# Optimization experiments

Measured on AMD Instinct MI355X. Metric: run time of the kernel, lower is better.

## Reference

```python
import jax, jax.numpy as jnp
import numpy as np

E, H, L = 1280, 20, 8192
D = E // H


def setup_inputs() -> dict:
    key = jax.random.key(0)
    ks = jax.random.split(key, 12)
    inp = {
        "hidden_states": jax.random.normal(ks[0], (1, 1, E), jnp.float32),
        "position_ids": jax.random.randint(ks[1], (1,), 0, L, jnp.int64),
        "k_cache": jax.random.normal(ks[2], (1, H, L, D), jnp.float32),
        "v_cache": jax.random.normal(ks[3], (1, H, L, D), jnp.float32),
        "Wq": jax.random.normal(ks[4], (E, E), jnp.float32) * 0.02,
        "bq": jax.random.normal(ks[5], (E,), jnp.float32) * 0.02,
        "Wk": jax.random.normal(ks[6], (E, E), jnp.float32) * 0.02,
        "Wv": jax.random.normal(ks[7], (E, E), jnp.float32) * 0.02,
        "bv": jax.random.normal(ks[8], (E,), jnp.float32) * 0.02,
        "Wo": jax.random.normal(ks[9], (E, E), jnp.float32) * 0.02,
        "bo": jax.random.normal(ks[10], (E,), jnp.float32) * 0.02,
    }
    return inp


def reference(hidden_states, position_ids, k_cache, v_cache, Wq, bq, Wk, Wv, bv, Wo, bo):
    # hidden_states: [1,1,E]; k_cache/v_cache: [1,H,L,D]; position_ids: [1] int
    h = k_cache.shape[1]
    d = k_cache.shape[3]
    l = k_cache.shape[2]
    e = h * d
    scale = jnp.asarray(d, hidden_states.dtype) ** -0.5

    def split_heads(x):  # [1,1,E] -> [1,H,1,D]
        return x.reshape(1, 1, h, d).transpose(0, 2, 1, 3)

    q = split_heads((hidden_states @ Wq.T + bq) * scale)
    k_new = split_heads(hidden_states @ Wk.T)          # k_proj has no bias
    v_new = split_heads(hidden_states @ Wv.T + bv)

    pos = position_ids.reshape(())
    positions = jnp.arange(l)
    write_mask = (positions == pos)[None, None, :, None]   # [1,1,L,1]
    # masked broadcast-update of the KV cache (same math as cache*(1-m)+new*m)
    new_k_cache = jnp.where(write_mask, k_new, k_cache)    # [1,H,L,D]
    new_v_cache = jnp.where(write_mask, v_new, v_cache)

    scores = jnp.einsum('bhqd,bhkd->bhqk', q, new_k_cache)  # [1,H,1,L]
    causal = jnp.where(positions[None, None, None, :] <= pos,
                       jnp.asarray(0.0, scores.dtype),
                       jnp.asarray(-1e9, scores.dtype))
    attn = jax.nn.softmax(scores + causal, axis=-1)
    out = jnp.einsum('bhqk,bhkd->bhqd', attn, new_v_cache)  # [1,H,1,D]
    out = out.transpose(0, 2, 1, 3).reshape(1, 1, e)
    out = out @ Wo.T + bo
    return out, new_k_cache, new_v_cache
```

## Files before the change

### kernel.cpp

```cpp
#include <hip/hip_runtime.h>

#define E 1280
#define H 20
#define L 8192
#define D 64
#define CHUNK 128
#define NCHUNK (L / CHUNK)

typedef float f4 __attribute__((ext_vector_type(4)));

__global__ void qkv_kernel(const float* __restrict__ hs,
                           const float* __restrict__ Wq, const float* __restrict__ bq,
                           const float* __restrict__ Wk,
                           const float* __restrict__ Wv, const float* __restrict__ bv,
                           float* __restrict__ qkv) {
    int row_global = blockIdx.x * 4 + (threadIdx.x >> 6);
    int lane = threadIdx.x & 63;
    int mat = row_global / E;
    int row = row_global - mat * E;
    const float* W = (mat == 0) ? Wq : (mat == 1) ? Wk : Wv;
    const float4* Wrow = (const float4*)(W + (size_t)row * E);
    const float4* h4 = (const float4*)hs;
    float sum = 0.f;
#pragma unroll
    for (int i = 0; i < 5; ++i) {
        int idx = lane + 64 * i;
        float4 w4 = Wrow[idx];
        float4 x4 = h4[idx];
        sum += w4.x * x4.x + w4.y * x4.y + w4.z * x4.z + w4.w * x4.w;
    }
#pragma unroll
    for (int off = 32; off > 0; off >>= 1) sum += __shfl_down(sum, off, 64);
    if (lane == 0) {
        float val;
        if (mat == 0)      val = (sum + bq[row]) * 0.125f;
        else if (mat == 1) val = sum;
        else               val = sum + bv[row];
        qkv[mat * E + row] = val;
    }
}

__global__ void kv_kernel(const float* __restrict__ kc, const float* __restrict__ vc,
                          const float* __restrict__ qkv, const int* __restrict__ pos_p,
                          float* __restrict__ out_k, float* __restrict__ out_v,
                          float* __restrict__ cmax, float* __restrict__ csum,
                          float* __restrict__ o_part) {
    int h = blockIdx.x / NCHUNK;
    int c = blockIdx.x - h * NCHUNK;
    int pos = pos_p[0];
    int tid = threadIdx.x;
    int wave = tid >> 6;
    int lane = tid & 63;
    int cc = tid & 15;
    int rg = tid >> 4;

    __shared__ float s_part[CHUNK][17];
    __shared__ float s_w[CHUNK];
    __shared__ float smax4[4];
    __shared__ float spsum[4];
    __shared__ float sacc[4][D];

    float4 q4  = ((const float4*)qkv)[h * 16 + cc];
    float4 kn4 = ((const float4*)(qkv + E))[h * 16 + cc];
    float4 vn4 = ((const float4*)(qkv + 2 * E))[h * 16 + cc];

    size_t base = ((size_t)h * L + (size_t)c * CHUNK) * D;
    const float* kbase = kc + base;
    const float* vbase = vc + base;
    float* okbase = out_k + base;
    float* ovbase = out_v + base;
    int l0 = c * CHUNK;

#pragma unroll
    for (int it = 0; it < CHUNK / 16; ++it) {
        int r = it * 16 + rg;
        int l = l0 + r;
        float4 k4 = ((const float4*)(kbase + r * D))[cc];
        if (l == pos) k4 = kn4;
        f4 kv = {k4.x, k4.y, k4.z, k4.w};
        __builtin_nontemporal_store(kv, (f4*)(okbase + r * D) + cc);
        s_part[r][cc] = k4.x * q4.x + k4.y * q4.y + k4.z * q4.z + k4.w * q4.w;
    }

    float4 vreg[CHUNK / 16];
#pragma unroll
    for (int it = 0; it < CHUNK / 16; ++it) {
        int r = it * 16 + rg;
        int l = l0 + r;
        float4 v4 = ((const float4*)(vbase + r * D))[cc];
        if (l == pos) v4 = vn4;
        f4 vv = {v4.x, v4.y, v4.z, v4.w};
        __builtin_nontemporal_store(vv, (f4*)(ovbase + r * D) + cc);
        vreg[it] = v4;
    }
    __syncthreads();

    float s = -INFINITY;
    if (tid < CHUNK) {
        float sum = 0.f;
#pragma unroll
        for (int i = 0; i < 16; ++i) sum += s_part[tid][i];
        s = (l0 + tid <= pos) ? sum : -INFINITY;
    }
    float lm = s;
#pragma unroll
    for (int off = 32; off > 0; off >>= 1)
        lm = fmaxf(lm, __shfl_xor(lm, off, 64));
    if (lane == 0) smax4[wave] = lm;
    __syncthreads();
    float m = fmaxf(fmaxf(smax4[0], smax4[1]), fmaxf(smax4[2], smax4[3]));

    float p = 0.f;
    if (tid < CHUNK) {
        p = (s > -1e30f) ? __expf(s - m) : 0.f;
        s_w[tid] = p;
    }
    float ps = p;
#pragma unroll
    for (int off = 32; off > 0; off >>= 1) ps += __shfl_xor(ps, off, 64);
    if (lane == 0) spsum[wave] = ps;
    __syncthreads();

    float4 acc = {0.f, 0.f, 0.f, 0.f};
#pragma unroll
    for (int it = 0; it < CHUNK / 16; ++it) {
        int r = it * 16 + rg;
        float w = s_w[r];
        acc.x += w * vreg[it].x; acc.y += w * vreg[it].y;
        acc.z += w * vreg[it].z; acc.w += w * vreg[it].w;
    }
    acc.x += __shfl_xor(acc.x, 16, 64); acc.y += __shfl_xor(acc.y, 16, 64);
    acc.z += __shfl_xor(acc.z, 16, 64); acc.w += __shfl_xor(acc.w, 16, 64);
    acc.x += __shfl_xor(acc.x, 32, 64); acc.y += __shfl_xor(acc.y, 32, 64);
    acc.z += __shfl_xor(acc.z, 32, 64); acc.w += __shfl_xor(acc.w, 32, 64);
    if ((lane >> 4) == 0) ((float4*)&sacc[wave][cc * 4])[0] = acc;
    __syncthreads();
    if (tid < D) {
        float o = sacc[0][tid] + sacc[1][tid] + sacc[2][tid] + sacc[3][tid];
        o_part[((size_t)h * NCHUNK + c) * D + tid] = o;
        if (tid == 0) {
            cmax[h * NCHUNK + c] = m;
            csum[h * NCHUNK + c] = spsum[0] + spsum[1] + spsum[2] + spsum[3];
        }
    }
}

__global__ void combine_kernel(const float* __restrict__ cmax, const float* __restrict__ csum,
                               const float* __restrict__ o_part, float* __restrict__ attn_out) {
    int h = blockIdx.x;
    int d = threadIdx.x;
    float m = -INFINITY;
#pragma unroll
    for (int c = 0; c < NCHUNK; ++c) m = fmaxf(m, cmax[h * NCHUNK + c]);
    float denom = 0.f, o = 0.f;
#pragma unroll 4
    for (int c = 0; c < NCHUNK; ++c) {
        float mc = cmax[h * NCHUNK + c];
        float sc = (mc > -1e30f) ? __expf(mc - m) : 0.f;
        denom += csum[h * NCHUNK + c] * sc;
        o += o_part[((size_t)h * NCHUNK + c) * D + d] * sc;
    }
    attn_out[h * D + d] = o / denom;
}

__global__ void ogemv_kernel(const float* __restrict__ attn_out, const float* __restrict__ Wo,
                             const float* __restrict__ bo, float* __restrict__ out) {
    int row = blockIdx.x * 4 + (threadIdx.x >> 6);
    int lane = threadIdx.x & 63;
    const float4* Wrow = (const float4*)(Wo + (size_t)row * E);
    const float4* x4 = (const float4*)attn_out;
    float sum = 0.f;
#pragma unroll
    for (int i = 0; i < 5; ++i) {
        int idx = lane + 64 * i;
        float4 w4 = Wrow[idx];
        float4 a4 = x4[idx];
        sum += w4.x * a4.x + w4.y * a4.y + w4.z * a4.z + w4.w * a4.w;
    }
#pragma unroll
    for (int off = 32; off > 0; off >>= 1) sum += __shfl_down(sum, off, 64);
    if (lane == 0) out[row] = sum + bo[row];
}

extern "C" void kernel_launch(void* const* d_in, const int* in_sizes, int n_in,
                              void* d_out, int out_size, void* d_ws, size_t ws_size,
                              hipStream_t stream) {
    const float* hs  = (const float*)d_in[0];
    const int*   pos = (const int*)d_in[1];
    const float* kc  = (const float*)d_in[2];
    const float* vc  = (const float*)d_in[3];
    const float* Wq  = (const float*)d_in[4];
    const float* bq  = (const float*)d_in[5];
    const float* Wk  = (const float*)d_in[6];
    const float* Wv  = (const float*)d_in[7];
    const float* bv  = (const float*)d_in[8];
    const float* Wo  = (const float*)d_in[9];
    const float* bo  = (const float*)d_in[10];

    float* out   = (float*)d_out;
    float* out_k = out + E;
    float* out_v = out_k + (size_t)H * L * D;

    float* ws       = (float*)d_ws;
    float* qkv      = ws;
    float* cmax     = qkv + 3 * E;
    float* csum     = cmax + H * NCHUNK;
    float* o_part   = csum + H * NCHUNK;
    float* attn_out = o_part + (size_t)H * NCHUNK * D;

    qkv_kernel<<<3 * E / 4, 256, 0, stream>>>(hs, Wq, bq, Wk, Wv, bv, qkv);
    kv_kernel<<<H * NCHUNK, 256, 0, stream>>>(kc, vc, qkv, pos, out_k, out_v,
                                              cmax, csum, o_part);
    combine_kernel<<<H, 64, 0, stream>>>(cmax, csum, o_part, attn_out);
    ogemv_kernel<<<E / 4, 256, 0, stream>>>(attn_out, Wo, bo, out);
}
```

Baseline: 45.23 us.

## Split KV cache copy into separate interleaved copy blocks within fused kernel

```diff
diff --git a/kernel.cpp b/kernel.cpp
--- a/kernel.cpp
+++ b/kernel.cpp
@@ -6,6 +6,11 @@
 #define D 64
 #define CHUNK 128
 #define NCHUNK (L / CHUNK)
+#define NF4_ARR (H * L * D / 4)
+#define NF4_TOT (2 * NF4_ARR)
+#define COPY_BLOCKS 1024
+#define COPY_STRIDE (COPY_BLOCKS * 256)
+#define COPY_ITERS (NF4_TOT / COPY_STRIDE)
 
 typedef float f4 __attribute__((ext_vector_type(4)));
 
@@ -40,14 +45,43 @@
     }
 }
 
-__global__ void kv_kernel(const float* __restrict__ kc, const float* __restrict__ vc,
-                          const float* __restrict__ qkv, const int* __restrict__ pos_p,
-                          float* __restrict__ out_k, float* __restrict__ out_v,
-                          float* __restrict__ cmax, float* __restrict__ csum,
-                          float* __restrict__ o_part) {
-    int h = blockIdx.x / NCHUNK;
-    int c = blockIdx.x - h * NCHUNK;
+__global__ void fused_kernel(const float* __restrict__ kc, const float* __restrict__ vc,
+                             const float* __restrict__ qkv, const int* __restrict__ pos_p,
+                             float* __restrict__ out_k, float* __restrict__ out_v,
+                             float* __restrict__ cmax, float* __restrict__ csum,
+                             float* __restrict__ o_part) {
     int pos = pos_p[0];
+    int g  = blockIdx.x / 9;
+    int rm = blockIdx.x - g * 9;
+
+    if (rm >= 5) {
+        int job = g * 4 + (rm - 5);
+        const f4* __restrict__ ksrc = (const f4*)kc;
+        const f4* __restrict__ vsrc = (const f4*)vc;
+        f4* __restrict__ kdst = (f4*)out_k;
+        f4* __restrict__ vdst = (f4*)out_v;
+        const f4* __restrict__ kn = (const f4*)(qkv + E);
+        const f4* __restrict__ vn = (const f4*)(qkv + 2 * E);
+        int t0 = job * 256 + threadIdx.x;
+#pragma unroll
+        for (int j = 0; j < COPY_ITERS; ++j) {
+            int idx = t0 + j * COPY_STRIDE;
+            bool isv = idx >= NF4_ARR;
+            int f = isv ? idx - NF4_ARR : idx;
+            f4 val = (isv ? vsrc : ksrc)[f];
+            int l = (f >> 4) & (L - 1);
+            if (l == pos) {
+                int h = f >> 17;
+                val = (isv ? vn : kn)[h * 16 + (f & 15)];
+            }
+            (isv ? vdst : kdst)[f] = val;
+        }
+        return;
+    }
+
+    int job = g * 5 + rm;
+    int h = job >> 6;
+    int c = job & (NCHUNK - 1);
     int tid = threadIdx.x;
     int wave = tid >> 6;
     int lane = tid & 63;
@@ -67,30 +101,18 @@
     size_t base = ((size_t)h * L + (size_t)c * CHUNK) * D;
     const float* kbase = kc + base;
     const float* vbase = vc + base;
-    float* okbase = out_k + base;
-    float* ovbase = out_v + base;
     int l0 = c * CHUNK;
 
+    float4 vreg[CHUNK / 16];
 #pragma unroll
     for (int it = 0; it < CHUNK / 16; ++it) {
         int r = it * 16 + rg;
         int l = l0 + r;
         float4 k4 = ((const float4*)(kbase + r * D))[cc];
         if (l == pos) k4 = kn4;
-        f4 kv = {k4.x, k4.y, k4.z, k4.w};
-        __builtin_nontemporal_store(kv, (f4*)(okbase + r * D) + cc);
         s_part[r][cc] = k4.x * q4.x + k4.y * q4.y + k4.z * q4.z + k4.w * q4.w;
-    }
-
-    float4 vreg[CHUNK / 16];
-#pragma unroll
-    for (int it = 0; it < CHUNK / 16; ++it) {
-        int r = it * 16 + rg;
-        int l = l0 + r;
         float4 v4 = ((const float4*)(vbase + r * D))[cc];
         if (l == pos) v4 = vn4;
-        f4 vv = {v4.x, v4.y, v4.z, v4.w};
-        __builtin_nontemporal_store(vv, (f4*)(ovbase + r * D) + cc);
         vreg[it] = v4;
     }
     __syncthreads();
@@ -209,8 +231,8 @@
     float* attn_out = o_part + (size_t)H * NCHUNK * D;
 
     qkv_kernel<<<3 * E / 4, 256, 0, stream>>>(hs, Wq, bq, Wk, Wv, bv, qkv);
-    kv_kernel<<<H * NCHUNK, 256, 0, stream>>>(kc, vc, qkv, pos, out_k, out_v,
-                                              cmax, csum, o_part);
+    fused_kernel<<<2304, 256, 0, stream>>>(kc, vc, qkv, pos, out_k, out_v,
+                                           cmax, csum, o_part);
     combine_kernel<<<H, 64, 0, stream>>>(cmax, csum, o_part, attn_out);
     ogemv_kernel<<<E / 4, 256, 0, stream>>>(attn_out, Wo, bo, out);
 }
```

After: 56.05 us. +23.9%, slower.
